# Performance work log

Measured on AMD Instinct MI355X. Metric: run time of the kernel, lower is better.

## Reference

```python
import jax, jax.numpy as jnp
import numpy as np
import math

B, S, D_MODEL, D_K = 4, 4096, 1024, 256

def setup_inputs() -> dict:
    key = jax.random.key(0)
    ks = jax.random.split(key, 9)
    def xavier(k, shape):
        fan_out, fan_in = shape
        limit = math.sqrt(6.0 / (fan_in + fan_out))
        return jax.random.uniform(k, shape, jnp.float32, -limit, limit)
    return {
        "_q": jax.random.normal(ks[0], (B, S, D_MODEL), jnp.float32),
        "_k": jax.random.normal(ks[1], (B, S, D_MODEL), jnp.float32),
        "_v": jax.random.normal(ks[2], (B, S, D_MODEL), jnp.float32),
        "mask": jnp.ones((B, 1, S), dtype=bool),  # unused by the original forward
        "Wq": xavier(ks[3], (D_K, D_MODEL)),
        "bq": jnp.zeros((D_K,), jnp.float32),
        "Wk": xavier(ks[4], (D_K, D_MODEL)),
        "bk": jnp.zeros((D_K,), jnp.float32),
        "Wv": xavier(ks[5], (D_K, D_MODEL)),
        "bv": jnp.zeros((D_K,), jnp.float32),
    }

def reference(_q, _k, _v, mask, Wq, bq, Wk, bk, Wv, bv):
    # Linear projections: x @ W.T + b  (torch nn.Linear semantics)
    q = jnp.einsum('bsm,km->bsk', _q, Wq) + bq  # [B,S,d_k]
    k = jnp.einsum('bsm,km->bsk', _k, Wk) + bk
    v = jnp.einsum('bsm,km->bsk', _v, Wv) + bv
    scores = jnp.einsum('bqk,bsk->bqs', q, k) / math.sqrt(D_K)  # [B,S,S]
    atten = jax.nn.softmax(scores, axis=-1)
    out = jnp.einsum('bqs,bsk->bqk', atten, v)  # [B,S,d_k]
    return out
```

## Files before the change

### kernel.cpp

```cpp
#include <hip/hip_runtime.h>
#include <stdint.h>

#define DEV static __device__ __forceinline__

typedef __bf16 bf16x8 __attribute__((ext_vector_type(8)));
typedef float f32x4 __attribute__((ext_vector_type(4)));

typedef const __attribute__((address_space(1))) void* as1cp;
typedef __attribute__((address_space(3))) void* as3p;

DEV uint32_t f2bf1(float f) {
  uint32_t u = __builtin_bit_cast(uint32_t, f);
  u += 0x7fffu + ((u >> 16) & 1u);
  return u >> 16;
}
DEV uint32_t f2bf2(float lo, float hi) { return f2bf1(lo) | (f2bf1(hi) << 16); }
DEV float bf2f(uint32_t h) { return __builtin_bit_cast(float, h << 16); }

DEV void gll16(const void* g, void* l) {
  __builtin_amdgcn_global_load_lds((as1cp)g, (as3p)l, 16, 0, 0);
}

__global__ __launch_bounds__(256, 3) void proj_kernel(
    const float* __restrict__ xq, const float* __restrict__ xk, const float* __restrict__ xv,
    const float* __restrict__ wq, const float* __restrict__ wk, const float* __restrict__ wv,
    const float* __restrict__ bq, const float* __restrict__ bk, const float* __restrict__ bv,
    uint16_t* __restrict__ qo, uint16_t* __restrict__ ko, uint16_t* __restrict__ vo)
{
  const int z = blockIdx.z;
  const float* X  = (z == 0) ? xq : (z == 1) ? xk : xv;
  const float* W  = (z == 0) ? wq : (z == 1) ? wk : wv;
  const float* Bi = (z == 0) ? bq : (z == 1) ? bk : bv;

  const int tid = threadIdx.x;
  const int lane = tid & 63;
  const int w = tid >> 6;
  const int wm = w >> 1, wn = w & 1;
  const int l15 = lane & 15, g = lane >> 4;
  const int m0 = blockIdx.x * 128;
  const int n0 = blockIdx.y * 128;

  __shared__ uint16_t sA[128 * 64];
  __shared__ uint16_t sB[128 * 64];

  const int am = tid >> 1, ak = (tid & 1) * 32;
  const float* Ap = X + (size_t)(m0 + am) * 1024 + ak;
  const float* Wp = W + (size_t)(n0 + am) * 1024 + ak;

  f32x4 acc[4][4];
  #pragma unroll
  for (int i = 0; i < 4; ++i)
    #pragma unroll
    for (int j = 0; j < 4; ++j) { f32x4 zz = {0.f, 0.f, 0.f, 0.f}; acc[i][j] = zz; }

  float ar[32];
  #pragma unroll
  for (int i = 0; i < 8; ++i) { float4 t = ((const float4*)Ap)[i];
    ar[4*i+0]=t.x; ar[4*i+1]=t.y; ar[4*i+2]=t.z; ar[4*i+3]=t.w; }

  const uint32_t ph = (uint32_t)(am * 128 + ak * 2) ^ ((uint32_t)(am & 7) << 4);

  for (int kt = 0; kt < 16; ++kt) {
    if (kt) __syncthreads();
    #pragma unroll
    for (int c = 0; c < 4; ++c) {
      uint4 p;
      p.x = f2bf2(ar[8*c+0], ar[8*c+1]); p.y = f2bf2(ar[8*c+2], ar[8*c+3]);
      p.z = f2bf2(ar[8*c+4], ar[8*c+5]); p.w = f2bf2(ar[8*c+6], ar[8*c+7]);
      *(uint4*)((char*)sA + (ph ^ (16u * c))) = p;
    }
    {
      float wr[32];
      const float* Wk = Wp + kt * 64;
      #pragma unroll
      for (int i = 0; i < 8; ++i) { float4 t = ((const float4*)Wk)[i];
        wr[4*i+0]=t.x; wr[4*i+1]=t.y; wr[4*i+2]=t.z; wr[4*i+3]=t.w; }
      #pragma unroll
      for (int c = 0; c < 4; ++c) {
        uint4 p;
        p.x = f2bf2(wr[8*c+0], wr[8*c+1]); p.y = f2bf2(wr[8*c+2], wr[8*c+3]);
        p.z = f2bf2(wr[8*c+4], wr[8*c+5]); p.w = f2bf2(wr[8*c+6], wr[8*c+7]);
        *(uint4*)((char*)sB + (ph ^ (16u * c))) = p;
      }
    }
    __syncthreads();
    if (kt < 15) {
      const float* Ap2 = Ap + (kt + 1) * 64;
      #pragma unroll
      for (int i = 0; i < 8; ++i) { float4 t = ((const float4*)Ap2)[i];
        ar[4*i+0]=t.x; ar[4*i+1]=t.y; ar[4*i+2]=t.z; ar[4*i+3]=t.w; }
    }
    #pragma unroll
    for (int ks = 0; ks < 2; ++ks) {
      bf16x8 fa[4], fb[4];
      #pragma unroll
      for (int f = 0; f < 4; ++f) {
        uint32_t row = wm * 64 + 16 * f + l15;
        fa[f] = *(const bf16x8*)((char*)sA + row * 128 +
                 (((uint32_t)(ks * 64 + g * 16)) ^ ((row & 7) << 4)));
      }
      #pragma unroll
      for (int f = 0; f < 4; ++f) {
        uint32_t row = wn * 64 + 16 * f + l15;
        fb[f] = *(const bf16x8*)((char*)sB + row * 128 +
                 (((uint32_t)(ks * 64 + g * 16)) ^ ((row & 7) << 4)));
      }
      #pragma unroll
      for (int fm = 0; fm < 4; ++fm)
        #pragma unroll
        for (int fn = 0; fn < 4; ++fn)
          acc[fm][fn] = __builtin_amdgcn_mfma_f32_16x16x32_bf16(fa[fm], fb[fn], acc[fm][fn], 0, 0, 0);
    }
  }

  #pragma unroll
  for (int fn = 0; fn < 4; ++fn) {
    const int n = n0 + wn * 64 + 16 * fn + l15;
    const float bias = Bi[n];
    #pragma unroll
    for (int fm = 0; fm < 4; ++fm) {
      const int mg = m0 + wm * 64 + 16 * fm + 4 * g;
      if (z == 0) {
        #pragma unroll
        for (int r = 0; r < 4; ++r)
          qo[(size_t)(mg + r) * 256 + n] =
              (uint16_t)f2bf1((acc[fm][fn][r] + bias) * 0.09016844f);
      } else if (z == 1) {
        #pragma unroll
        for (int r = 0; r < 4; ++r)
          ko[(size_t)(mg + r) * 256 + n] = (uint16_t)f2bf1(acc[fm][fn][r] + bias);
      } else {
        uint2 pv;
        pv.x = f2bf2(acc[fm][fn][0] + bias, acc[fm][fn][1] + bias);
        pv.y = f2bf2(acc[fm][fn][2] + bias, acc[fm][fn][3] + bias);
        *(uint2*)(vo + (((size_t)(mg >> 12)) << 20) + (((size_t)n) << 12) + (mg & 4095)) = pv;
      }
    }
  }
}

__global__ __launch_bounds__(512) void attn_kernel(
    const uint16_t* __restrict__ qg, const uint16_t* __restrict__ kg,
    const uint16_t* __restrict__ vg, float* __restrict__ out)
{
  extern __shared__ char smem[];

  const int bid = blockIdx.x;
  const int xcd = bid & 7, slot = bid >> 3;
  const int batch = xcd >> 1;
  const int q0 = (((xcd & 1) << 5) + slot) * 64;

  const int tid = threadIdx.x;
  const int lane = tid & 63;
  const int w = tid >> 6;
  const int hv = w >> 2;
  const int wq = w & 3;
  const int l15 = lane & 15, g = lane >> 4;
  const size_t rowb = (size_t)batch * 4096;

  bf16x8 qf[8];
  {
    const uint16_t* qp = qg + (rowb + q0 + wq * 16 + l15) * 256;
    #pragma unroll
    for (int ks = 0; ks < 8; ++ks) qf[ks] = *(const bf16x8*)(qp + ks * 32 + g * 8);
  }

  f32x4 o[16];
  #pragma unroll
  for (int i = 0; i < 16; ++i) { f32x4 zz = {0.f, 0.f, 0.f, 0.f}; o[i] = zz; }
  float mrow[4], lrow[4];
  #pragma unroll
  for (int r = 0; r < 4; ++r) { mrow[r] = -1e30f; lrow[r] = 0.f; }

  const char* kgb = (const char*)(kg + rowb * 256);
  const char* vgb = (const char*)(vg + (size_t)batch * 256 * 4096);

  auto STAGE = [&](int h, int buf, int t) {
    const int kv0 = (2 * t + h) * 32;
    char* kd = smem + (size_t)(h * 2 + buf) * 16384;
    char* vd = smem + 65536 + (size_t)(h * 2 + buf) * 16384;
    #pragma unroll
    for (int r2 = 0; r2 < 2; ++r2) {
      uint32_t L = (uint32_t)(tid + r2 * 512) * 16;
      uint32_t U = L ^ (((L >> 9) & 7u) << 4);
      gll16(kgb + (size_t)(kv0 + (U >> 9)) * 512 + (U & 511), kd + L);
      uint32_t d = L >> 6;
      uint32_t kvo = (L >> 4) & 3u;
      gll16(vgb + (size_t)d * 8192 + (size_t)(kv0 + 8 * kvo) * 2, vd + L);
    }
  };

  STAGE(0, 0, 0); STAGE(1, 0, 0);
  char* Pw = smem + 131072 + (size_t)w * 1024;
  int buf = 0;

  for (int t = 0; t < 64; ++t) {
    __syncthreads();
    if (t + 1 < 64) { STAGE(0, buf ^ 1, t + 1); STAGE(1, buf ^ 1, t + 1); }

    const char* Kb = smem + (size_t)(hv * 2 + buf) * 16384;
    const char* Vb = smem + 65536 + (size_t)(hv * 2 + buf) * 16384;

    f32x4 s4[2];
    #pragma unroll
    for (int f = 0; f < 2; ++f) { f32x4 zz = {0.f, 0.f, 0.f, 0.f}; s4[f] = zz; }
    #pragma unroll
    for (int ks = 0; ks < 8; ++ks) {
      bf16x8 kf[2];
      #pragma unroll
      for (int f = 0; f < 2; ++f) {
        uint32_t row = 16 * f + l15;
        kf[f] = *(const bf16x8*)(Kb + row * 512 +
                 (((uint32_t)(ks * 64 + g * 16)) ^ ((l15 & 7) << 4)));
      }
      #pragma unroll
      for (int f = 0; f < 2; ++f)
        s4[f] = __builtin_amdgcn_mfma_f32_16x16x32_bf16(qf[ks], kf[f], s4[f], 0, 0, 0);
    }

    float mx[4];
    #pragma unroll
    for (int r = 0; r < 4; ++r) {
      float m2 = fmaxf(s4[0][r], s4[1][r]);
      m2 = fmaxf(m2, __shfl_xor(m2, 1, 64));
      m2 = fmaxf(m2, __shfl_xor(m2, 2, 64));
      m2 = fmaxf(m2, __shfl_xor(m2, 4, 64));
      m2 = fmaxf(m2, __shfl_xor(m2, 8, 64));
      mx[r] = m2;
    }
    int stable = (mx[0] <= mrow[0] + 8.f) && (mx[1] <= mrow[1] + 8.f) &&
                 (mx[2] <= mrow[2] + 8.f) && (mx[3] <= mrow[3] + 8.f);
    if (!__all(stable)) {
      float sc[4];
      #pragma unroll
      for (int r = 0; r < 4; ++r) {
        float mn = fmaxf(mrow[r], mx[r]);
        sc[r] = exp2f(mrow[r] - mn);
        mrow[r] = mn;
        lrow[r] *= sc[r];
      }
      #pragma unroll
      for (int j = 0; j < 16; ++j)
        #pragma unroll
        for (int r = 0; r < 4; ++r) o[j][r] *= sc[r];
    }
    float ps[2][4];
    #pragma unroll
    for (int r = 0; r < 4; ++r) {
      float sum = 0.f;
      #pragma unroll
      for (int f = 0; f < 2; ++f) { ps[f][r] = exp2f(s4[f][r] - mrow[r]); sum += ps[f][r]; }
      sum += __shfl_xor(sum, 1, 64);
      sum += __shfl_xor(sum, 2, 64);
      sum += __shfl_xor(sum, 4, 64);
      sum += __shfl_xor(sum, 8, 64);
      lrow[r] += sum;
    }

    #pragma unroll
    for (int f = 0; f < 2; ++f)
      #pragma unroll
      for (int r = 0; r < 4; ++r)
        *(uint16_t*)(Pw + (4 * g + r) * 64 +
            (((uint32_t)(32 * f + 2 * l15)) ^ ((uint32_t)g << 4))) = (uint16_t)f2bf1(ps[f][r]);

    bf16x8 pa = *(const bf16x8*)(Pw + l15 * 64 + 16 * (g ^ (l15 >> 2)));
    #pragma unroll
    for (int fd = 0; fd < 16; ++fd) {
      bf16x8 vbf = *(const bf16x8*)(Vb + fd * 1024 + l15 * 64 + g * 16);
      o[fd] = __builtin_amdgcn_mfma_f32_16x16x32_bf16(pa, vbf, o[fd], 0, 0, 0);
    }

    buf ^= 1;
  }

  float*    mlb = (float*)smem;
  uint32_t* ob  = (uint32_t*)(smem + 8192);
  __syncthreads();
  if (hv == 1) {
    #pragma unroll
    for (int r = 0; r < 4; ++r) {
      mlb[((0 * 4 + wq) * 64 + lane) * 4 + r] = mrow[r];
      mlb[((1 * 4 + wq) * 64 + lane) * 4 + r] = lrow[r];
    }
    #pragma unroll
    for (int fd = 0; fd < 16; ++fd)
      #pragma unroll
      for (int p = 0; p < 2; ++p)
        ob[(wq * 32 + fd * 2 + p) * 64 + lane] = f2bf2(o[fd][2 * p], o[fd][2 * p + 1]);
  }
  __syncthreads();
  if (hv == 0) {
    float a[4], b2[4], inv[4];
    #pragma unroll
    for (int r = 0; r < 4; ++r) {
      float mu = mlb[((0 * 4 + wq) * 64 + lane) * 4 + r];
      float lu = mlb[((1 * 4 + wq) * 64 + lane) * 4 + r];
      float mn = fmaxf(mrow[r], mu);
      a[r]  = exp2f(mrow[r] - mn);
      b2[r] = exp2f(mu - mn);
      inv[r] = 1.f / (lrow[r] * a[r] + lu * b2[r]);
    }
    float* op = out + (rowb + q0 + wq * 16) * 256;
    #pragma unroll
    for (int fd = 0; fd < 16; ++fd) {
      #pragma unroll
      for (int p = 0; p < 2; ++p) {
        uint32_t u = ob[(wq * 32 + fd * 2 + p) * 64 + lane];
        float vlo = bf2f(u & 0xffffu), vhi = bf2f(u >> 16);
        int r0 = 2 * p, r1 = 2 * p + 1;
        op[(4 * g + r0) * 256 + 16 * fd + l15] =
            (o[fd][r0] * a[r0] + vlo * b2[r0]) * inv[r0];
        op[(4 * g + r1) * 256 + 16 * fd + l15] =
            (o[fd][r1] * a[r1] + vhi * b2[r1]) * inv[r1];
      }
    }
  }
}

extern "C" void kernel_launch(void* const* d_in, const int* in_sizes, int n_in,
                              void* d_out, int out_size, void* d_ws, size_t ws_size,
                              hipStream_t stream) {
  const float* xq = (const float*)d_in[0];
  const float* xk = (const float*)d_in[1];
  const float* xv = (const float*)d_in[2];
  const float* wq = (const float*)d_in[4];
  const float* bq = (const float*)d_in[5];
  const float* wk = (const float*)d_in[6];
  const float* bk = (const float*)d_in[7];
  const float* wv = (const float*)d_in[8];
  const float* bv = (const float*)d_in[9];

  uint16_t* qws = (uint16_t*)d_ws;
  uint16_t* kws = qws + (size_t)4 * 4096 * 256;
  uint16_t* vws = kws + (size_t)4 * 4096 * 256;

  proj_kernel<<<dim3(128, 2, 3), 256, 0, stream>>>(
      xq, xk, xv, wq, wk, wv, bq, bk, bv, qws, kws, vws);

  (void)hipFuncSetAttribute((const void*)attn_kernel,
                            hipFuncAttributeMaxDynamicSharedMemorySize, 139264);
  attn_kernel<<<dim3(256), 512, 139264, stream>>>(qws, kws, vws, (float*)d_out);
}
```

Measured before the change: 446.6 us.

## Coalesce projection loads, use native bf16 conversion, precompute attention staging offsets

The projection kernel now loads its A and W tiles so that 16 threads read consecutive float4s of one row across 8 row groups, instead of each thread reading 32 contiguous floats. This is meant to improve global load coalescing. The manual round-to-nearest bf16 conversion is replaced with a native __bf16 cast, which may lower to hardware convert instructions. The attention kernel precomputes its K/V global_load_lds offsets outside the loop and remaps the V staging layout so each lane reads 16 contiguous bytes, which cuts per-iteration address arithmetic.

After: 435.0 us. 1.03x faster.

```diff
diff --git a/kernel.cpp b/kernel.cpp
--- a/kernel.cpp
+++ b/kernel.cpp
@@ -9,12 +9,12 @@
 typedef const __attribute__((address_space(1))) void* as1cp;
 typedef __attribute__((address_space(3))) void* as3p;
 
-DEV uint32_t f2bf1(float f) {
-  uint32_t u = __builtin_bit_cast(uint32_t, f);
-  u += 0x7fffu + ((u >> 16) & 1u);
-  return u >> 16;
-}
-DEV uint32_t f2bf2(float lo, float hi) { return f2bf1(lo) | (f2bf1(hi) << 16); }
+DEV uint32_t pk2(float lo, float hi) {
+  uint16_t a = __builtin_bit_cast(uint16_t, (__bf16)lo);
+  uint16_t b = __builtin_bit_cast(uint16_t, (__bf16)hi);
+  return (uint32_t)a | ((uint32_t)b << 16);
+}
+DEV uint16_t bfc(float f) { return __builtin_bit_cast(uint16_t, (__bf16)f); }
 DEV float bf2f(uint32_t h) { return __builtin_bit_cast(float, h << 16); }
 
 DEV void gll16(const void* g, void* l) {
@@ -43,9 +43,16 @@
   __shared__ uint16_t sA[128 * 64];
   __shared__ uint16_t sB[128 * 64];
 
-  const int am = tid >> 1, ak = (tid & 1) * 32;
-  const float* Ap = X + (size_t)(m0 + am) * 1024 + ak;
-  const float* Wp = W + (size_t)(n0 + am) * 1024 + ak;
+  const int srow = tid >> 4;
+  const int scu  = tid & 15;
+  const float* Abase = X + (size_t)(m0 + srow) * 1024 + scu * 4;
+  const float* Wbase = W + (size_t)(n0 + srow) * 1024 + scu * 4;
+  uint32_t sdst[8];
+  #pragma unroll
+  for (int r = 0; r < 8; ++r) {
+    uint32_t row = (uint32_t)(r * 16 + srow);
+    sdst[r] = row * 128 + (((uint32_t)scu * 8) ^ ((row & 7) << 4));
+  }
 
   f32x4 acc[4][4];
   #pragma unroll
@@ -53,42 +60,34 @@
     #pragma unroll
     for (int j = 0; j < 4; ++j) { f32x4 zz = {0.f, 0.f, 0.f, 0.f}; acc[i][j] = zz; }
 
-  float ar[32];
-  #pragma unroll
-  for (int i = 0; i < 8; ++i) { float4 t = ((const float4*)Ap)[i];
-    ar[4*i+0]=t.x; ar[4*i+1]=t.y; ar[4*i+2]=t.z; ar[4*i+3]=t.w; }
-
-  const uint32_t ph = (uint32_t)(am * 128 + ak * 2) ^ ((uint32_t)(am & 7) << 4);
+  float4 a4[8];
+  #pragma unroll
+  for (int r = 0; r < 8; ++r)
+    a4[r] = *(const float4*)(Abase + (size_t)r * 16384);
 
   for (int kt = 0; kt < 16; ++kt) {
     if (kt) __syncthreads();
     #pragma unroll
-    for (int c = 0; c < 4; ++c) {
-      uint4 p;
-      p.x = f2bf2(ar[8*c+0], ar[8*c+1]); p.y = f2bf2(ar[8*c+2], ar[8*c+3]);
-      p.z = f2bf2(ar[8*c+4], ar[8*c+5]); p.w = f2bf2(ar[8*c+6], ar[8*c+7]);
-      *(uint4*)((char*)sA + (ph ^ (16u * c))) = p;
+    for (int r = 0; r < 8; ++r) {
+      uint2 p; p.x = pk2(a4[r].x, a4[r].y); p.y = pk2(a4[r].z, a4[r].w);
+      *(uint2*)((char*)sA + sdst[r]) = p;
     }
     {
-      float wr[32];
-      const float* Wk = Wp + kt * 64;
-      #pragma unroll
-      for (int i = 0; i < 8; ++i) { float4 t = ((const float4*)Wk)[i];
-        wr[4*i+0]=t.x; wr[4*i+1]=t.y; wr[4*i+2]=t.z; wr[4*i+3]=t.w; }
-      #pragma unroll
-      for (int c = 0; c < 4; ++c) {
-        uint4 p;
-        p.x = f2bf2(wr[8*c+0], wr[8*c+1]); p.y = f2bf2(wr[8*c+2], wr[8*c+3]);
-        p.z = f2bf2(wr[8*c+4], wr[8*c+5]); p.w = f2bf2(wr[8*c+6], wr[8*c+7]);
-        *(uint4*)((char*)sB + (ph ^ (16u * c))) = p;
+      float4 w4[8];
+      #pragma unroll
+      for (int r = 0; r < 8; ++r)
+        w4[r] = *(const float4*)(Wbase + (size_t)r * 16384 + kt * 64);
+      #pragma unroll
+      for (int r = 0; r < 8; ++r) {
+        uint2 p; p.x = pk2(w4[r].x, w4[r].y); p.y = pk2(w4[r].z, w4[r].w);
+        *(uint2*)((char*)sB + sdst[r]) = p;
       }
     }
     __syncthreads();
     if (kt < 15) {
-      const float* Ap2 = Ap + (kt + 1) * 64;
-      #pragma unroll
-      for (int i = 0; i < 8; ++i) { float4 t = ((const float4*)Ap2)[i];
-        ar[4*i+0]=t.x; ar[4*i+1]=t.y; ar[4*i+2]=t.z; ar[4*i+3]=t.w; }
+      #pragma unroll
+      for (int r = 0; r < 8; ++r)
+        a4[r] = *(const float4*)(Abase + (size_t)r * 16384 + (kt + 1) * 64);
     }
     #pragma unroll
     for (int ks = 0; ks < 2; ++ks) {
@@ -124,15 +123,15 @@
         #pragma unroll
         for (int r = 0; r < 4; ++r)
           qo[(size_t)(mg + r) * 256 + n] =
-              (uint16_t)f2bf1((acc[fm][fn][r] + bias) * 0.09016844f);
+              bfc((acc[fm][fn][r] + bias) * 0.09016844f);
       } else if (z == 1) {
         #pragma unroll
         for (int r = 0; r < 4; ++r)
-          ko[(size_t)(mg + r) * 256 + n] = (uint16_t)f2bf1(acc[fm][fn][r] + bias);
+          ko[(size_t)(mg + r) * 256 + n] = bfc(acc[fm][fn][r] + bias);
       } else {
         uint2 pv;
-        pv.x = f2bf2(acc[fm][fn][0] + bias, acc[fm][fn][1] + bias);
-        pv.y = f2bf2(acc[fm][fn][2] + bias, acc[fm][fn][3] + bias);
+        pv.x = pk2(acc[fm][fn][0] + bias, acc[fm][fn][1] + bias);
+        pv.y = pk2(acc[fm][fn][2] + bias, acc[fm][fn][3] + bias);
         *(uint2*)(vo + (((size_t)(mg >> 12)) << 20) + (((size_t)n) << 12) + (mg & 4095)) = pv;
       }
     }
@@ -175,31 +174,47 @@
   const char* kgb = (const char*)(kg + rowb * 256);
   const char* vgb = (const char*)(vg + (size_t)batch * 256 * 4096);
 
-  auto STAGE = [&](int h, int buf, int t) {
-    const int kv0 = (2 * t + h) * 32;
-    char* kd = smem + (size_t)(h * 2 + buf) * 16384;
-    char* vd = smem + 65536 + (size_t)(h * 2 + buf) * 16384;
-    #pragma unroll
-    for (int r2 = 0; r2 < 2; ++r2) {
-      uint32_t L = (uint32_t)(tid + r2 * 512) * 16;
-      uint32_t U = L ^ (((L >> 9) & 7u) << 4);
-      gll16(kgb + (size_t)(kv0 + (U >> 9)) * 512 + (U & 511), kd + L);
-      uint32_t d = L >> 6;
-      uint32_t kvo = (L >> 4) & 3u;
-      gll16(vgb + (size_t)d * 8192 + (size_t)(kv0 + 8 * kvo) * 2, vd + L);
+  uint32_t kOff[2][2], vOff[2][2], dOff[2];
+  #pragma unroll
+  for (int i = 0; i < 2; ++i) {
+    uint32_t L = (uint32_t)(i * 512 + tid) * 16;
+    dOff[i] = L;
+    uint32_t row = L >> 9;
+    uint32_t colsw = (L & 511) ^ ((row & 7) << 4);
+    uint32_t fd = L >> 10, g2 = (L >> 8) & 3, lv = (L >> 4) & 15;
+    #pragma unroll
+    for (int h = 0; h < 2; ++h) {
+      kOff[h][i] = (h * 32 + row) * 512 + colsw;
+      vOff[h][i] = (fd * 16 + lv) * 8192 + (h * 32 + g2 * 8) * 2;
+    }
+  }
+
+  auto STAGE = [&](int buf, int t) {
+    const char* kt_ = kgb + (size_t)t * 32768;
+    const char* vt_ = vgb + (size_t)t * 128;
+    #pragma unroll
+    for (int h = 0; h < 2; ++h) {
+      char* kd = smem + (size_t)(h * 2 + buf) * 16384;
+      char* vd = smem + 65536 + (size_t)(h * 2 + buf) * 16384;
+      #pragma unroll
+      for (int i = 0; i < 2; ++i) {
+        gll16(kt_ + kOff[h][i], kd + dOff[i]);
+        gll16(vt_ + vOff[h][i], vd + dOff[i]);
+      }
     }
   };
 
-  STAGE(0, 0, 0); STAGE(1, 0, 0);
+  STAGE(0, 0);
+  int buf = 0;
+  const int hb = hv * 2;
   char* Pw = smem + 131072 + (size_t)w * 1024;
-  int buf = 0;
 
   for (int t = 0; t < 64; ++t) {
     __syncthreads();
-    if (t + 1 < 64) { STAGE(0, buf ^ 1, t + 1); STAGE(1, buf ^ 1, t + 1); }
-
-    const char* Kb = smem + (size_t)(hv * 2 + buf) * 16384;
-    const char* Vb = smem + 65536 + (size_t)(hv * 2 + buf) * 16384;
+    if (t + 1 < 64) STAGE(buf ^ 1, t + 1);
+
+    const char* Kb = smem + (size_t)(hb + buf) * 16384;
+    const char* Vb = smem + 65536 + (size_t)(hb + buf) * 16384;
 
     f32x4 s4[2];
     #pragma unroll
@@ -262,12 +277,12 @@
       #pragma unroll
       for (int r = 0; r < 4; ++r)
         *(uint16_t*)(Pw + (4 * g + r) * 64 +
-            (((uint32_t)(32 * f + 2 * l15)) ^ ((uint32_t)g << 4))) = (uint16_t)f2bf1(ps[f][r]);
+            (((uint32_t)(32 * f + 2 * l15)) ^ ((uint32_t)g << 4))) = bfc(ps[f][r]);
 
     bf16x8 pa = *(const bf16x8*)(Pw + l15 * 64 + 16 * (g ^ (l15 >> 2)));
     #pragma unroll
     for (int fd = 0; fd < 16; ++fd) {
-      bf16x8 vbf = *(const bf16x8*)(Vb + fd * 1024 + l15 * 64 + g * 16);
+      bf16x8 vbf = *(const bf16x8*)(Vb + fd * 1024 + lane * 16);
       o[fd] = __builtin_amdgcn_mfma_f32_16x16x32_bf16(pa, vbf, o[fd], 0, 0, 0);
     }
 
@@ -287,7 +302,7 @@
     for (int fd = 0; fd < 16; ++fd)
       #pragma unroll
       for (int p = 0; p < 2; ++p)
-        ob[(wq * 32 + fd * 2 + p) * 64 + lane] = f2bf2(o[fd][2 * p], o[fd][2 * p + 1]);
+        ob[(wq * 32 + fd * 2 + p) * 64 + lane] = pk2(o[fd][2 * p], o[fd][2 * p + 1]);
   }
   __syncthreads();
   if (hv == 0) {
```
